# Kernel tuning notes

Hardware: AMD Instinct MI355X
Metric: run time of the kernel (lower is better)

The kernel has to match this reference:

```python
import jax, jax.numpy as jnp
import numpy as np

NUM_EXPERTS = 4096
NUM_KEYS = 64  # floor(sqrt(num_experts))
TOP_K = 16
NORM_TOPK = False
BN_EPS = 1e-5


def setup_inputs() -> dict:
    key = jax.random.key(0)
    ks = jax.random.split(key, 7)
    B, S, H, I = 2, 2048, 2048, 8192
    s = 0.02
    return {
        "hidden_states": jax.random.normal(ks[0], (B, S, H), jnp.float32),
        "router_gate_w": jax.random.normal(ks[1], (2 * NUM_KEYS, H), jnp.float32) * s,
        "down_embed": jax.random.normal(ks[2], (NUM_EXPERTS, H), jnp.float32) * s,
        "up_embed": jax.random.normal(ks[3], (NUM_EXPERTS, H), jnp.float32) * s,
        "gate_w": jax.random.normal(ks[4], (I, H), jnp.float32) * s,
        "up_w": jax.random.normal(ks[5], (I, H), jnp.float32) * s,
        "down_w": jax.random.normal(ks[6], (H, I), jnp.float32) * s,
    }


def reference(hidden_states, router_gate_w, down_embed, up_embed, gate_w, up_w, down_w):
    B, S, H = hidden_states.shape
    x = hidden_states.reshape(-1, H)  # [N, H]

    # BatchNorm1d(affine=False), training-mode batch statistics (biased var)
    mu = jnp.mean(x, axis=0, keepdims=True)
    var = jnp.mean(jnp.square(x - mu), axis=0, keepdims=True)
    xn = (x - mu) * jax.lax.rsqrt(var + BN_EPS)

    # product-key router: logits [2, N, num_keys]
    rlog = (xn @ router_gate_w.T).reshape(-1, 2, NUM_KEYS).transpose(1, 0, 2)
    logp = jax.nn.log_softmax(rlog, axis=-1)

    # full product scores [N, nk, nk]; top-k over nk*nk candidates
    full = logp[0][:, :, None] + logp[1][:, None, :]
    scores, indices = jax.lax.top_k(full.reshape(-1, NUM_KEYS * NUM_KEYS), TOP_K)
    routing_weights = jnp.exp(scores)  # [N, k]
    if NORM_TOPK:
        routing_weights = routing_weights / jnp.sum(routing_weights, axis=-1, keepdims=True)

    # PEER-style expert: scalar key match then weighted up-embedding sum
    d = down_embed[indices]  # [N, k, H]
    u = up_embed[indices]    # [N, k, H]
    h = jnp.einsum('nh,nkh->nk', x, d)
    experts_states = jnp.einsum('nk,nk,nkh->nh', routing_weights, h, u)

    # dense gated MLP (silu)
    mlp = (jax.nn.silu(x @ gate_w.T) * (x @ up_w.T)) @ down_w.T

    out = (mlp + experts_states).reshape(B, S, H)
    return out, rlog
```

## Files before the change

kernel.cpp:

```cpp
#include <hip/hip_runtime.h>
#include <stdint.h>

#define H_DIM 2048
#define N_TOK 4096
#define I_DIM 8192

typedef __attribute__((ext_vector_type(8))) short short8;
typedef __attribute__((ext_vector_type(4))) float f32x4;

typedef const __attribute__((address_space(1))) unsigned int* gp_t;
typedef __attribute__((address_space(3))) unsigned int* lp_t;

__device__ __forceinline__ void gload16(const unsigned short* g, short* l) {
    __builtin_amdgcn_global_load_lds((gp_t)g, (lp_t)l, 16, 0, 0);
}

__device__ __forceinline__ unsigned short f2bf(float f) {
    union { float f; unsigned int u; } c; c.f = f;
    unsigned int u = c.u;
    return (unsigned short)((u + 0x7FFFu + ((u >> 16) & 1u)) >> 16);
}
__device__ __forceinline__ float bf2f(unsigned short u) {
    union { unsigned int i; float f; } c; c.i = ((unsigned int)u) << 16;
    return c.f;
}

__device__ __forceinline__ float wmax64(float v) {
#pragma unroll
    for (int o = 32; o > 0; o >>= 1) v = fmaxf(v, __shfl_xor(v, o));
    return v;
}
__device__ __forceinline__ float wsum64(float v) {
#pragma unroll
    for (int o = 32; o > 0; o >>= 1) v += __shfl_xor(v, o);
    return v;
}

template<int K, int RSTEP, int LSTEP>
__device__ __forceinline__ void stage4(const unsigned short* src, short* dst) {
#pragma unroll
    for (int j = 0; j < 4; ++j)
        gload16(src + (size_t)j * RSTEP * K, dst + j * LSTEP);
}

__global__ __launch_bounds__(256) void bn_stats(const float* __restrict__ x,
                                                float* __restrict__ ps, float* __restrict__ pq) {
    int col = blockIdx.x * 256 + threadIdx.x;
    int r0  = blockIdx.y * 128;
    float s = 0.f, q = 0.f;
    for (int r = 0; r < 128; ++r) {
        float v = x[(size_t)(r0 + r) * H_DIM + col];
        s += v; q += v * v;
    }
    ps[blockIdx.y * H_DIM + col] = s;
    pq[blockIdx.y * H_DIM + col] = q;
}

__global__ __launch_bounds__(256) void bn_finalize(const float* __restrict__ ps, const float* __restrict__ pq,
                                                   float* __restrict__ mu, float* __restrict__ rsig) {
    int c = blockIdx.x * 256 + threadIdx.x;
    float s = 0.f, q = 0.f;
    for (int i = 0; i < 32; ++i) { s += ps[i * H_DIM + c]; q += pq[i * H_DIM + c]; }
    float m = s * (1.f / N_TOK);
    float v = q * (1.f / N_TOK) - m * m;
    mu[c] = m;
    rsig[c] = rsqrtf(v + 1e-5f);
}

__global__ __launch_bounds__(256) void cvt_all(const float* __restrict__ gw, const float* __restrict__ uw,
                                               const float* __restrict__ dw, const float* __restrict__ de,
                                               const float* __restrict__ ue, const float* __restrict__ x,
                                               unsigned short* __restrict__ gwb, unsigned short* __restrict__ uwb,
                                               unsigned short* __restrict__ dwb, unsigned short* __restrict__ deb,
                                               unsigned short* __restrict__ ueb, unsigned short* __restrict__ xb) {
    int b = blockIdx.x;
    const float* src; unsigned short* dst; size_t base;
    if      (b < 8192)  { src = gw; dst = gwb; base = (size_t)b; }
    else if (b < 16384) { src = uw; dst = uwb; base = (size_t)(b - 8192); }
    else if (b < 24576) { src = dw; dst = dwb; base = (size_t)(b - 16384); }
    else if (b < 28672) { src = de; dst = deb; base = (size_t)(b - 24576); }
    else if (b < 32768) { src = ue; dst = ueb; base = (size_t)(b - 28672); }
    else                { src = x;  dst = xb;  base = (size_t)(b - 32768); }
    size_t off = (base * 256 + threadIdx.x) * 8;
    float4 a = *(const float4*)(src + off);
    float4 c = *(const float4*)(src + off + 4);
    short8 s;
    s[0]=(short)f2bf(a.x); s[1]=(short)f2bf(a.y); s[2]=(short)f2bf(a.z); s[3]=(short)f2bf(a.w);
    s[4]=(short)f2bf(c.x); s[5]=(short)f2bf(c.y); s[6]=(short)f2bf(c.z); s[7]=(short)f2bf(c.w);
    *(short8*)(dst + off) = s;
}

__global__ __launch_bounds__(256) void cvt_x(const float* __restrict__ x, unsigned short* __restrict__ xb) {
    size_t i = ((size_t)blockIdx.x * 256 + threadIdx.x) * 4;
    float4 v = *(const float4*)(x + i);
    uint2 o;
    o.x = (unsigned)f2bf(v.x) | ((unsigned)f2bf(v.y) << 16);
    o.y = (unsigned)f2bf(v.z) | ((unsigned)f2bf(v.w) << 16);
    *(uint2*)(xb + i) = o;
}

__global__ __launch_bounds__(256) void cvt_w(const float* __restrict__ src, unsigned short* __restrict__ dst) {
    size_t off = ((size_t)blockIdx.x * 256 + threadIdx.x) * 8;
    float4 a = *(const float4*)(src + off);
    float4 b = *(const float4*)(src + off + 4);
    short8 s;
    s[0]=(short)f2bf(a.x); s[1]=(short)f2bf(a.y); s[2]=(short)f2bf(a.z); s[3]=(short)f2bf(a.w);
    s[4]=(short)f2bf(b.x); s[5]=(short)f2bf(b.y); s[6]=(short)f2bf(b.z); s[7]=(short)f2bf(b.w);
    *(short8*)(dst + off) = s;
}

__global__ __launch_bounds__(256) void router_kernel(const float* __restrict__ x, const float* __restrict__ rgw,
                                                     const float* __restrict__ mu, const float* __restrict__ rsig,
                                                     float* __restrict__ rlog) {
    __shared__ float xs[16][65];
    __shared__ float rs[128][65];
    const int t = threadIdx.x;
    const int n0 = blockIdx.x * 16;
    const int tk = t >> 5;
    const int jj = t & 31;
    float acc[2][4] = {{0.f,0.f,0.f,0.f},{0.f,0.f,0.f,0.f}};

    for (int kc = 0; kc < H_DIM; kc += 64) {
        {
            int row = t >> 4, c4 = (t & 15) * 4;
            float4 v = *(const float4*)(x + (size_t)(n0 + row) * H_DIM + kc + c4);
            float4 m = *(const float4*)(mu + kc + c4);
            float4 r = *(const float4*)(rsig + kc + c4);
            xs[row][c4 + 0] = (v.x - m.x) * r.x;
            xs[row][c4 + 1] = (v.y - m.y) * r.y;
            xs[row][c4 + 2] = (v.z - m.z) * r.z;
            xs[row][c4 + 3] = (v.w - m.w) * r.w;
        }
        {
            int row = t >> 1, base = (t & 1) * 32;
            const float* src = rgw + (size_t)row * H_DIM + kc + base;
#pragma unroll
            for (int i = 0; i < 8; ++i) {
                float4 v = *(const float4*)(src + i * 4);
                rs[row][base + i*4 + 0] = v.x;
                rs[row][base + i*4 + 1] = v.y;
                rs[row][base + i*4 + 2] = v.z;
                rs[row][base + i*4 + 3] = v.w;
            }
        }
        __syncthreads();
#pragma unroll 4
        for (int k = 0; k < 64; ++k) {
            float x0 = xs[tk][k], x1 = xs[tk + 8][k];
            float r0 = rs[jj][k], r1 = rs[jj + 32][k], r2 = rs[jj + 64][k], r3 = rs[jj + 96][k];
            acc[0][0] += x0 * r0; acc[0][1] += x0 * r1; acc[0][2] += x0 * r2; acc[0][3] += x0 * r3;
            acc[1][0] += x1 * r0; acc[1][1] += x1 * r1; acc[1][2] += x1 * r2; acc[1][3] += x1 * r3;
        }
        __syncthreads();
    }
#pragma unroll
    for (int a = 0; a < 2; ++a)
#pragma unroll
        for (int b = 0; b < 4; ++b) {
            int n = n0 + tk + 8 * a;
            int j = jj + 32 * b;
            rlog[(size_t)(j >> 6) * (N_TOK * 64) + (size_t)n * 64 + (j & 63)] = acc[a][b];
        }
}

__global__ __launch_bounds__(256) void topk_kernel(const float* __restrict__ rlog,
                                                   float* __restrict__ topw, int* __restrict__ topi) {
    const int lane = threadIdx.x & 63;
    const int n = blockIdx.x * 4 + (threadIdx.x >> 6);

    float a = rlog[(size_t)n * 64 + lane];
    float b = rlog[(size_t)(N_TOK * 64) + (size_t)n * 64 + lane];
    float ma = wmax64(a);
    float lpa = a - ma - logf(wsum64(expf(a - ma)));
    float mb = wmax64(b);
    float lpb = b - mb - logf(wsum64(expf(b - mb)));

    float va = lpa, vb = lpb;
    float tva = -1e30f, tvb = -1e30f; int tia = 0, tib = 0;
    for (int it = 0; it < 16; ++it) {
        float mx = wmax64(va);
        int w = __ffsll(__ballot(va == mx)) - 1;
        if (lane == it) { tva = mx; tia = w; }
        if (lane == w) va = -1e30f;
        mx = wmax64(vb);
        w = __ffsll(__ballot(vb == mx)) - 1;
        if (lane == it) { tvb = mx; tib = w; }
        if (lane == w) vb = -1e30f;
    }
    float av = __shfl(tva, lane >> 2);
    int   ai = __shfl(tia, lane >> 2);
    int   q0 = (lane & 3) * 4;
    float c0 = av + __shfl(tvb, q0 + 0); int b0 = __shfl(tib, q0 + 0);
    float c1 = av + __shfl(tvb, q0 + 1); int b1 = __shfl(tib, q0 + 1);
    float c2 = av + __shfl(tvb, q0 + 2); int b2 = __shfl(tib, q0 + 2);
    float c3 = av + __shfl(tvb, q0 + 3); int b3 = __shfl(tib, q0 + 3);

    for (int it = 0; it < 16; ++it) {
        float lv = c0; int lq = 0;
        if (c1 > lv) { lv = c1; lq = 1; }
        if (c2 > lv) { lv = c2; lq = 2; }
        if (c3 > lv) { lv = c3; lq = 3; }
        float mx = wmax64(lv);
        int w = __ffsll(__ballot(lv == mx)) - 1;
        if (lane == w) {
            int bj;
            switch (lq) {
                case 0:  bj = b0; c0 = -1e30f; break;
                case 1:  bj = b1; c1 = -1e30f; break;
                case 2:  bj = b2; c2 = -1e30f; break;
                default: bj = b3; c3 = -1e30f; break;
            }
            topw[n * 16 + it] = expf(mx);
            topi[n * 16 + it] = ai * 64 + bj;
        }
    }
}

__global__ __launch_bounds__(256) void experts_kernel_b(const float* __restrict__ x, const unsigned short* __restrict__ de,
                                                        const unsigned short* __restrict__ ue, const float* __restrict__ topw,
                                                        const int* __restrict__ topi, float* __restrict__ out) {
    __shared__ float psum[16][4];
    const int n = blockIdx.x;
    const int t = threadIdx.x, lane = t & 63, wid = t >> 6;

    float xr[8];
    {
        float4 v0 = *(const float4*)(x + (size_t)n * H_DIM + t * 8);
        float4 v1 = *(const float4*)(x + (size_t)n * H_DIM + t * 8 + 4);
        xr[0]=v0.x; xr[1]=v0.y; xr[2]=v0.z; xr[3]=v0.w;
        xr[4]=v1.x; xr[5]=v1.y; xr[6]=v1.z; xr[7]=v1.w;
    }
    int   eidx[16];
    float ew[16];
#pragma unroll
    for (int k = 0; k < 16; ++k) { eidx[k] = topi[n * 16 + k]; ew[k] = topw[n * 16 + k]; }

#pragma unroll
    for (int k = 0; k < 16; ++k) {
        short8 d = *(const short8*)(de + (size_t)eidx[k] * H_DIM + t * 8);
        float p = 0.f;
#pragma unroll
        for (int j = 0; j < 8; ++j) p += bf2f((unsigned short)d[j]) * xr[j];
        p = wsum64(p);
        if (lane == 0) psum[k][wid] = p;
    }
    __syncthreads();

    float acc[8] = {0,0,0,0,0,0,0,0};
#pragma unroll
    for (int k = 0; k < 16; ++k) {
        float h = psum[k][0] + psum[k][1] + psum[k][2] + psum[k][3];
        float coef = ew[k] * h;
        short8 u = *(const short8*)(ue + (size_t)eidx[k] * H_DIM + t * 8);
#pragma unroll
        for (int j = 0; j < 8; ++j) acc[j] += coef * bf2f((unsigned short)u[j]);
    }
    float4 o0 = {acc[0], acc[1], acc[2], acc[3]};
    float4 o1 = {acc[4], acc[5], acc[6], acc[7]};
    *(float4*)(out + (size_t)n * H_DIM + t * 8)     = o0;
    *(float4*)(out + (size_t)n * H_DIM + t * 8 + 4) = o1;
}

__global__ __launch_bounds__(256) void experts_kernel(const float* __restrict__ x, const float* __restrict__ de,
                                                      const float* __restrict__ ue, const float* __restrict__ topw,
                                                      const int* __restrict__ topi, float* __restrict__ out) {
    __shared__ float psum[16][4];
    const int n = blockIdx.x;
    const int t = threadIdx.x, lane = t & 63, wid = t >> 6;

    float xr[8];
    {
        float4 v0 = *(const float4*)(x + (size_t)n * H_DIM + t * 8);
        float4 v1 = *(const float4*)(x + (size_t)n * H_DIM + t * 8 + 4);
        xr[0]=v0.x; xr[1]=v0.y; xr[2]=v0.z; xr[3]=v0.w;
        xr[4]=v1.x; xr[5]=v1.y; xr[6]=v1.z; xr[7]=v1.w;
    }
    int   eidx[16];
    float ew[16];
#pragma unroll
    for (int k = 0; k < 16; ++k) { eidx[k] = topi[n * 16 + k]; ew[k] = topw[n * 16 + k]; }

#pragma unroll
    for (int k = 0; k < 16; ++k) {
        const float* dr = de + (size_t)eidx[k] * H_DIM + t * 8;
        float4 v0 = *(const float4*)dr;
        float4 v1 = *(const float4*)(dr + 4);
        float p = v0.x*xr[0] + v0.y*xr[1] + v0.z*xr[2] + v0.w*xr[3]
                + v1.x*xr[4] + v1.y*xr[5] + v1.z*xr[6] + v1.w*xr[7];
        p = wsum64(p);
        if (lane == 0) psum[k][wid] = p;
    }
    __syncthreads();

    float acc[8] = {0,0,0,0,0,0,0,0};
#pragma unroll
    for (int k = 0; k < 16; ++k) {
        float h = psum[k][0] + psum[k][1] + psum[k][2] + psum[k][3];
        float coef = ew[k] * h;
        const float* ur = ue + (size_t)eidx[k] * H_DIM + t * 8;
        float4 v0 = *(const float4*)ur;
        float4 v1 = *(const float4*)(ur + 4);
        acc[0] += coef * v0.x; acc[1] += coef * v0.y; acc[2] += coef * v0.z; acc[3] += coef * v0.w;
        acc[4] += coef * v1.x; acc[5] += coef * v1.y; acc[6] += coef * v1.z; acc[7] += coef * v1.w;
    }
    float4 o0 = {acc[0], acc[1], acc[2], acc[3]};
    float4 o1 = {acc[4], acc[5], acc[6], acc[7]};
    *(float4*)(out + (size_t)n * H_DIM + t * 8)     = o0;
    *(float4*)(out + (size_t)n * H_DIM + t * 8 + 4) = o1;
}

#define SWZB(row, byteoff) ((byteoff) ^ (((row) & 7) << 4))

#define NT256 (H_DIM / 64)

__global__ __launch_bounds__(512, 2) void gemm256(const unsigned short* __restrict__ Amat,
                                                  const unsigned short* __restrict__ Bmat,
                                                  unsigned short* __restrict__ act, int mode) {
    __shared__ __attribute__((aligned(16))) short sA[2][16384];
    __shared__ __attribute__((aligned(16))) short sB[2][16384];
    const int t = threadIdx.x;
    const int lane = t & 63, wid = t >> 6;
    const int wm = wid >> 2, wn = wid & 3;
    const int l15 = lane & 15, l4 = lane >> 4;
    const int bid = blockIdx.x;
    const int sw = (bid & 7) * 64 + (bid >> 3);
    const int bx = sw & 31, by = sw >> 5;
    const int row0 = by * 256, col0 = bx * 256;

    const int rseg = lane >> 3;
    const int chunk = (lane & 7) ^ rseg;
    const unsigned short* aSrc = Amat + (size_t)(row0 + wid * 8 + rseg) * H_DIM + chunk * 8;
    const unsigned short* bSrc = Bmat + (size_t)(col0 + wid * 8 + rseg) * H_DIM + chunk * 8;

    const int swzb = (l15 & 7) << 4;
    const int kx0 = (l4 * 16) ^ swzb;
    const int kx1 = (64 + l4 * 16) ^ swzb;
    const int arow = (wm * 128 + l15) * 64;
    const int brow = (wn * 64 + l15) * 64;

    f32x4 zero = {0.f, 0.f, 0.f, 0.f};
    f32x4 acc[8][4];
#pragma unroll
    for (int m = 0; m < 8; ++m)
#pragma unroll
        for (int n = 0; n < 4; ++n) acc[m][n] = zero;

    stage4<H_DIM, 64, 4096>(aSrc, &sA[0][wid * 512]);
    stage4<H_DIM, 64, 4096>(bSrc, &sB[0][wid * 512]);
    __syncthreads();

    int cur = 0;
    for (int g = 0; g < NT256; ++g) {
        if (g + 1 < NT256) {
            stage4<H_DIM, 64, 4096>(aSrc + (size_t)(g + 1) * 64, &sA[cur ^ 1][wid * 512]);
            stage4<H_DIM, 64, 4096>(bSrc + (size_t)(g + 1) * 64, &sB[cur ^ 1][wid * 512]);
        }
        const short* Ac = &sA[cur][0];
        const short* Bc = &sB[cur][0];
        {
            short8 a0[4], a0h[4], b0[4];
#pragma unroll
            for (int m = 0; m < 4; ++m) a0[m]  = *(const short8*)(Ac + arow + m * 1024 + (kx0 >> 1));
#pragma unroll
            for (int m = 0; m < 4; ++m) a0h[m] = *(const short8*)(Ac + arow + (m + 4) * 1024 + (kx0 >> 1));
#pragma unroll
            for (int n = 0; n < 4; ++n) b0[n]  = *(const short8*)(Bc + brow + n * 1024 + (kx0 >> 1));
            __builtin_amdgcn_s_setprio(1);
#pragma unroll
            for (int m = 0; m < 4; ++m)
#pragma unroll
                for (int n = 0; n < 4; ++n)
                    acc[m][n] = __builtin_amdgcn_mfma_f32_16x16x32_bf16(a0[m], b0[n], acc[m][n], 0, 0, 0);
#pragma unroll
            for (int m = 0; m < 4; ++m)
#pragma unroll
                for (int n = 0; n < 4; ++n)
                    acc[m + 4][n] = __builtin_amdgcn_mfma_f32_16x16x32_bf16(a0h[m], b0[n], acc[m + 4][n], 0, 0, 0);
            __builtin_amdgcn_s_setprio(0);
        }
        {
            short8 a1[4], a1h[4], b1[4];
#pragma unroll
            for (int m = 0; m < 4; ++m) a1[m]  = *(const short8*)(Ac + arow + m * 1024 + (kx1 >> 1));
#pragma unroll
            for (int m = 0; m < 4; ++m) a1h[m] = *(const short8*)(Ac + arow + (m + 4) * 1024 + (kx1 >> 1));
#pragma unroll
            for (int n = 0; n < 4; ++n) b1[n]  = *(const short8*)(Bc + brow + n * 1024 + (kx1 >> 1));
            __builtin_amdgcn_s_setprio(1);
#pragma unroll
            for (int m = 0; m < 4; ++m)
#pragma unroll
                for (int n = 0; n < 4; ++n)
                    acc[m][n] = __builtin_amdgcn_mfma_f32_16x16x32_bf16(a1[m], b1[n], acc[m][n], 0, 0, 0);
#pragma unroll
            for (int m = 0; m < 4; ++m)
#pragma unroll
                for (int n = 0; n < 4; ++n)
                    acc[m + 4][n] = __builtin_amdgcn_mfma_f32_16x16x32_bf16(a1h[m], b1[n], acc[m + 4][n], 0, 0, 0);
            __builtin_amdgcn_s_setprio(0);
        }
        __syncthreads();
        cur ^= 1;
    }

    const int rbase = row0 + wm * 128, cbase = col0 + wn * 64;
    if (mode == 0) {
#pragma unroll
        for (int m = 0; m < 8; ++m)
#pragma unroll
            for (int n = 0; n < 4; ++n)
#pragma unroll
                for (int j = 0; j < 4; ++j) {
                    int r = rbase + m * 16 + l4 * 4 + j;
                    int c2 = cbase + n * 16 + l15;
                    act[(size_t)r * I_DIM + c2] = f2bf(acc[m][n][j]);
                }
    } else {
#pragma unroll
        for (int m = 0; m < 8; ++m)
#pragma unroll
            for (int n = 0; n < 4; ++n)
#pragma unroll
                for (int j = 0; j < 4; ++j) {
                    int r = rbase + m * 16 + l4 * 4 + j;
                    int c2 = cbase + n * 16 + l15;
                    size_t idx = (size_t)r * I_DIM + c2;
                    float gv = bf2f(act[idx]);
                    float uv = acc[m][n][j];
                    float sv = gv / (1.f + expf(-gv));
                    act[idx] = f2bf(sv * uv);
                }
    }
}

#define NTD (I_DIM / 64)

__global__ __launch_bounds__(256, 2) void gemm_down128(const unsigned short* __restrict__ act,
                                                       const unsigned short* __restrict__ dwb,
                                                       float* __restrict__ out) {
    __shared__ __attribute__((aligned(16))) short sA[2][8192];
    __shared__ __attribute__((aligned(16))) short sB[2][8192];
    const int t = threadIdx.x;
    const int lane = t & 63, wid = t >> 6;
    const int wm = wid >> 1, wn = wid & 1;
    const int l15 = lane & 15, l4 = lane >> 4;
    const int bid = blockIdx.x;
    const int sw = (bid & 7) * 64 + (bid >> 3);
    const int bx = sw & 15, by = sw >> 4;
    const int row0 = by * 128, col0 = bx * 128;

    const int rseg = lane >> 3;
    const int chunk = (lane & 7) ^ rseg;
    const unsigned short* aSrc = act + (size_t)(row0 + wid * 8 + rseg) * I_DIM + chunk * 8;
    const unsigned short* bSrc = dwb + (size_t)(col0 + wid * 8 + rseg) * I_DIM + chunk * 8;

    const int swzb = (l15 & 7) << 4;
    const int kx0 = (l4 * 16) ^ swzb;
    const int kx1 = (64 + l4 * 16) ^ swzb;
    const int arow = (wm * 64 + l15) * 64;
    const int brow = (wn * 64 + l15) * 64;

    f32x4 zero = {0.f, 0.f, 0.f, 0.f};
    f32x4 acc[4][4];
#pragma unroll
    for (int m = 0; m < 4; ++m)
#pragma unroll
        for (int n = 0; n < 4; ++n) acc[m][n] = zero;

    stage4<I_DIM, 32, 2048>(aSrc, &sA[0][wid * 512]);
    stage4<I_DIM, 32, 2048>(bSrc, &sB[0][wid * 512]);
    __syncthreads();

    int cur = 0;
    for (int g = 0; g < NTD; ++g) {
        if (g + 1 < NTD) {
            stage4<I_DIM, 32, 2048>(aSrc + (size_t)(g + 1) * 64, &sA[cur ^ 1][wid * 512]);
            stage4<I_DIM, 32, 2048>(bSrc + (size_t)(g + 1) * 64, &sB[cur ^ 1][wid * 512]);
        }
        const short* Ac = &sA[cur][0];
        const short* Bc = &sB[cur][0];
        {
            short8 a0[4], b0[4];
#pragma unroll
            for (int m = 0; m < 4; ++m) a0[m] = *(const short8*)(Ac + arow + m * 1024 + (kx0 >> 1));
#pragma unroll
            for (int n = 0; n < 4; ++n) b0[n] = *(const short8*)(Bc + brow + n * 1024 + (kx0 >> 1));
            __builtin_amdgcn_s_setprio(1);
#pragma unroll
            for (int m = 0; m < 4; ++m)
#pragma unroll
                for (int n = 0; n < 4; ++n)
                    acc[m][n] = __builtin_amdgcn_mfma_f32_16x16x32_bf16(a0[m], b0[n], acc[m][n], 0, 0, 0);
            __builtin_amdgcn_s_setprio(0);
        }
        {
            short8 a1[4], b1[4];
#pragma unroll
            for (int m = 0; m < 4; ++m) a1[m] = *(const short8*)(Ac + arow + m * 1024 + (kx1 >> 1));
#pragma unroll
            for (int n = 0; n < 4; ++n) b1[n] = *(const short8*)(Bc + brow + n * 1024 + (kx1 >> 1));
            __builtin_amdgcn_s_setprio(1);
#pragma unroll
            for (int m = 0; m < 4; ++m)
#pragma unroll
                for (int n = 0; n < 4; ++n)
                    acc[m][n] = __builtin_amdgcn_mfma_f32_16x16x32_bf16(a1[m], b1[n], acc[m][n], 0, 0, 0);
            __builtin_amdgcn_s_setprio(0);
        }
        __syncthreads();
        cur ^= 1;
    }

    const int rbase = row0 + wm * 64, cbase = col0 + wn * 64;
#pragma unroll
    for (int m = 0; m < 4; ++m)
#pragma unroll
        for (int n = 0; n < 4; ++n)
#pragma unroll
            for (int j = 0; j < 4; ++j) {
                int r = rbase + m * 16 + l4 * 4 + j;
                int c2 = cbase + n * 16 + l15;
                out[(size_t)r * H_DIM + c2] += acc[m][n][j];
            }
}

__global__ __launch_bounds__(256) void gemm_gu(const unsigned short* __restrict__ xb,
                                               const float* __restrict__ gw, const float* __restrict__ uw,
                                               unsigned short* __restrict__ act) {
    __shared__ __attribute__((aligned(16))) short As[128 * 64];
    __shared__ __attribute__((aligned(16))) short Bg[128 * 64];
    __shared__ __attribute__((aligned(16))) short Bu[128 * 64];
    const int t = threadIdx.x;
    const int lane = t & 63, wid = t >> 6;
    const int wr = wid >> 1, wc = wid & 1;
    const int l15 = lane & 15, l4 = lane >> 4;
    const int row0 = blockIdx.y * 128;
    const int col0 = blockIdx.x * 128;
    const int srow = t >> 1, shalf = (t & 1) * 32;

    f32x4 zero = {0.f, 0.f, 0.f, 0.f};
    f32x4 accg[4][4], accu[4][4];
#pragma unroll
    for (int m = 0; m < 4; ++m)
#pragma unroll
        for (int n = 0; n < 4; ++n) { accg[m][n] = zero; accu[m][n] = zero; }

    for (int kt = 0; kt < H_DIM; kt += 64) {
        {
            const unsigned short* src = xb + (size_t)(row0 + srow) * H_DIM + kt + shalf;
#pragma unroll
            for (int i = 0; i < 4; ++i) {
                int boff = SWZB(srow, (shalf + i * 8) * 2);
                *(short8*)(As + srow * 64 + (boff >> 1)) = *(const short8*)(src + i * 8);
            }
        }
        {
            const float* g = gw + (size_t)(col0 + srow) * H_DIM + kt + shalf;
            const float* u = uw + (size_t)(col0 + srow) * H_DIM + kt + shalf;
#pragma unroll
            for (int i = 0; i < 4; ++i) {
                int boff = SWZB(srow, (shalf + i * 8) * 2);
                float4 a0 = *(const float4*)(g + i * 8);
                float4 a1 = *(const float4*)(g + i * 8 + 4);
                short8 s;
                s[0]=(short)f2bf(a0.x); s[1]=(short)f2bf(a0.y); s[2]=(short)f2bf(a0.z); s[3]=(short)f2bf(a0.w);
                s[4]=(short)f2bf(a1.x); s[5]=(short)f2bf(a1.y); s[6]=(short)f2bf(a1.z); s[7]=(short)f2bf(a1.w);
                *(short8*)(Bg + srow * 64 + (boff >> 1)) = s;
                float4 b0 = *(const float4*)(u + i * 8);
                float4 b1 = *(const float4*)(u + i * 8 + 4);
                short8 r;
                r[0]=(short)f2bf(b0.x); r[1]=(short)f2bf(b0.y); r[2]=(short)f2bf(b0.z); r[3]=(short)f2bf(b0.w);
                r[4]=(short)f2bf(b1.x); r[5]=(short)f2bf(b1.y); r[6]=(short)f2bf(b1.z); r[7]=(short)f2bf(b1.w);
                *(short8*)(Bu + srow * 64 + (boff >> 1)) = r;
            }
        }
        __syncthreads();
#pragma unroll
        for (int kk = 0; kk < 64; kk += 32) {
            short8 af[4], bgf[4], buf_[4];
#pragma unroll
            for (int m = 0; m < 4; ++m) {
                int row = wr * 64 + m * 16 + l15;
                af[m] = *(const short8*)(As + row * 64 + (SWZB(row, (kk + l4 * 8) * 2) >> 1));
            }
#pragma unroll
            for (int n = 0; n < 4; ++n) {
                int row = wc * 64 + n * 16 + l15;
                int off = row * 64 + (SWZB(row, (kk + l4 * 8) * 2) >> 1);
                bgf[n]  = *(const short8*)(Bg + off);
                buf_[n] = *(const short8*)(Bu + off);
            }
#pragma unroll
            for (int m = 0; m < 4; ++m)
#pragma unroll
                for (int n = 0; n < 4; ++n) {
                    accg[m][n] = __builtin_amdgcn_mfma_f32_16x16x32_bf16(af[m], bgf[n],  accg[m][n], 0, 0, 0);
                    accu[m][n] = __builtin_amdgcn_mfma_f32_16x16x32_bf16(af[m], buf_[n], accu[m][n], 0, 0, 0);
                }
        }
        __syncthreads();
    }
    const int rbase = row0 + wr * 64, cbase = col0 + wc * 64;
#pragma unroll
    for (int m = 0; m < 4; ++m)
#pragma unroll
        for (int n = 0; n < 4; ++n)
#pragma unroll
            for (int j = 0; j < 4; ++j) {
                int r = rbase + m * 16 + l4 * 4 + j;
                int c = cbase + n * 16 + l15;
                float gv = accg[m][n][j];
                float uv = accu[m][n][j];
                float sv = gv / (1.f + expf(-gv));
                act[(size_t)r * I_DIM + c] = f2bf(sv * uv);
            }
}

__global__ __launch_bounds__(256) void gemm_down(const unsigned short* __restrict__ act,
                                                 const float* __restrict__ dw, float* __restrict__ out) {
    __shared__ __attribute__((aligned(16))) short As[128 * 64];
    __shared__ __attribute__((aligned(16))) short Bs[128 * 64];
    const int t = threadIdx.x;
    const int lane = t & 63, wid = t >> 6;
    const int wr = wid >> 1, wc = wid & 1;
    const int l15 = lane & 15, l4 = lane >> 4;
    const int row0 = blockIdx.y * 128;
    const int col0 = blockIdx.x * 128;
    const int srow = t >> 1, shalf = (t & 1) * 32;

    f32x4 zero = {0.f, 0.f, 0.f, 0.f};
    f32x4 acc[4][4];
#pragma unroll
    for (int m = 0; m < 4; ++m)
#pragma unroll
        for (int n = 0; n < 4; ++n) acc[m][n] = zero;

    for (int kt = 0; kt < I_DIM; kt += 64) {
        {
            const unsigned short* src = act + (size_t)(row0 + srow) * I_DIM + kt + shalf;
#pragma unroll
            for (int i = 0; i < 4; ++i) {
                int boff = SWZB(srow, (shalf + i * 8) * 2);
                *(short8*)(As + srow * 64 + (boff >> 1)) = *(const short8*)(src + i * 8);
            }
        }
        {
            const float* g = dw + (size_t)(col0 + srow) * I_DIM + kt + shalf;
#pragma unroll
            for (int i = 0; i < 4; ++i) {
                int boff = SWZB(srow, (shalf + i * 8) * 2);
                float4 a0 = *(const float4*)(g + i * 8);
                float4 a1 = *(const float4*)(g + i * 8 + 4);
                short8 s;
                s[0]=(short)f2bf(a0.x); s[1]=(short)f2bf(a0.y); s[2]=(short)f2bf(a0.z); s[3]=(short)f2bf(a0.w);
                s[4]=(short)f2bf(a1.x); s[5]=(short)f2bf(a1.y); s[6]=(short)f2bf(a1.z); s[7]=(short)f2bf(a1.w);
                *(short8*)(Bs + srow * 64 + (boff >> 1)) = s;
            }
        }
        __syncthreads();
#pragma unroll
        for (int kk = 0; kk < 64; kk += 32) {
            short8 af[4], bf[4];
#pragma unroll
            for (int m = 0; m < 4; ++m) {
                int row = wr * 64 + m * 16 + l15;
                af[m] = *(const short8*)(As + row * 64 + (SWZB(row, (kk + l4 * 8) * 2) >> 1));
            }
#pragma unroll
            for (int n = 0; n < 4; ++n) {
                int row = wc * 64 + n * 16 + l15;
                bf[n] = *(const short8*)(Bs + row * 64 + (SWZB(row, (kk + l4 * 8) * 2) >> 1));
            }
#pragma unroll
            for (int m = 0; m < 4; ++m)
#pragma unroll
                for (int n = 0; n < 4; ++n)
                    acc[m][n] = __builtin_amdgcn_mfma_f32_16x16x32_bf16(af[m], bf[n], acc[m][n], 0, 0, 0);
        }
        __syncthreads();
    }
    const int rbase = row0 + wr * 64, cbase = col0 + wc * 64;
#pragma unroll
    for (int m = 0; m < 4; ++m)
#pragma unroll
        for (int n = 0; n < 4; ++n)
#pragma unroll
            for (int j = 0; j < 4; ++j) {
                int r = rbase + m * 16 + l4 * 4 + j;
                int c = cbase + n * 16 + l15;
                out[(size_t)r * H_DIM + c] += acc[m][n][j];
            }
}

extern "C" void kernel_launch(void* const* d_in, const int* in_sizes, int n_in,
                              void* d_out, int out_size, void* d_ws, size_t ws_size,
                              hipStream_t stream) {
    const float* x   = (const float*)d_in[0];
    const float* rgw = (const float*)d_in[1];
    const float* de  = (const float*)d_in[2];
    const float* ue  = (const float*)d_in[3];
    const float* gw  = (const float*)d_in[4];
    const float* uw  = (const float*)d_in[5];
    const float* dw  = (const float*)d_in[6];
    float* out = (float*)d_out;
    char* ws = (char*)d_ws;

    float* ps   = (float*)(ws + 0);
    float* pq   = (float*)(ws + 262144);
    float* mu   = (float*)(ws + 524288);
    float* rsig = (float*)(ws + 532480);
    float* topw = (float*)(ws + 540672);
    int*   topi = (int*)  (ws + 802816);
    unsigned short* xb  = (unsigned short*)(ws + 1179648);
    unsigned short* act = (unsigned short*)(ws + 17956864);
    unsigned short* gwb = (unsigned short*)(ws + 85065728);
    unsigned short* uwb = (unsigned short*)(ws + 118620160);
    unsigned short* dwb = (unsigned short*)(ws + 152174592);
    unsigned short* deb = (unsigned short*)(ws + 185729024);
    unsigned short* ueb = (unsigned short*)(ws + 202506240);
    float* rlog = out + 8388608;
    const bool fast  = ws_size >= 185729024ULL;
    const bool fast2 = ws_size >= 219283456ULL;

    bn_stats   <<<dim3(8, 32), 256, 0, stream>>>(x, ps, pq);
    bn_finalize<<<8, 256, 0, stream>>>(ps, pq, mu, rsig);
    router_kernel<<<256, 256, 0, stream>>>(x, rgw, mu, rsig, rlog);
    topk_kernel<<<1024, 256, 0, stream>>>(rlog, topw, topi);

    if (fast2) {
        cvt_all<<<36864, 256, 0, stream>>>(gw, uw, dw, de, ue, x, gwb, uwb, dwb, deb, ueb, xb);
        experts_kernel_b<<<4096, 256, 0, stream>>>(x, deb, ueb, topw, topi, out);
        gemm256<<<512, 512, 0, stream>>>(xb, gwb, act, 0);
        gemm256<<<512, 512, 0, stream>>>(xb, uwb, act, 1);
        gemm_down128<<<512, 256, 0, stream>>>(act, dwb, out);
    } else if (fast) {
        cvt_x<<<8192, 256, 0, stream>>>(x, xb);
        cvt_w<<<8192, 256, 0, stream>>>(gw, gwb);
        cvt_w<<<8192, 256, 0, stream>>>(uw, uwb);
        cvt_w<<<8192, 256, 0, stream>>>(dw, dwb);
        experts_kernel<<<4096, 256, 0, stream>>>(x, de, ue, topw, topi, out);
        gemm256<<<512, 512, 0, stream>>>(xb, gwb, act, 0);
        gemm256<<<512, 512, 0, stream>>>(xb, uwb, act, 1);
        gemm_down128<<<512, 256, 0, stream>>>(act, dwb, out);
    } else {
        cvt_x<<<8192, 256, 0, stream>>>(x, xb);
        experts_kernel<<<4096, 256, 0, stream>>>(x, de, ue, topw, topi, out);
        gemm_gu  <<<dim3(64, 32), 256, 0, stream>>>(xb, gw, uw, act);
        gemm_down<<<dim3(16, 32), 256, 0, stream>>>(act, dw, out);
    }
}
```

Measured before the change: 768.9 us.

## Fuse gate and up GEMMs into one kernel with SiLU epilogue

```diff
diff --git a/kernel.cpp b/kernel.cpp
--- a/kernel.cpp
+++ b/kernel.cpp
@@ -40,6 +40,12 @@
 __device__ __forceinline__ void stage4(const unsigned short* src, short* dst) {
 #pragma unroll
     for (int j = 0; j < 4; ++j)
+        gload16(src + (size_t)j * RSTEP * K, dst + j * LSTEP);
+}
+template<int K, int RSTEP, int LSTEP>
+__device__ __forceinline__ void stage2(const unsigned short* src, short* dst) {
+#pragma unroll
+    for (int j = 0; j < 2; ++j)
         gload16(src + (size_t)j * RSTEP * K, dst + j * LSTEP);
 }
 
@@ -311,126 +317,112 @@
 
 #define SWZB(row, byteoff) ((byteoff) ^ (((row) & 7) << 4))
 
-#define NT256 (H_DIM / 64)
-
-__global__ __launch_bounds__(512, 2) void gemm256(const unsigned short* __restrict__ Amat,
-                                                  const unsigned short* __restrict__ Bmat,
-                                                  unsigned short* __restrict__ act, int mode) {
+#define NTGU (H_DIM / 64)
+
+__global__ __launch_bounds__(512, 2) void gemm_gu256(const unsigned short* __restrict__ xb,
+                                                     const unsigned short* __restrict__ gwb,
+                                                     const unsigned short* __restrict__ uwb,
+                                                     unsigned short* __restrict__ act) {
     __shared__ __attribute__((aligned(16))) short sA[2][16384];
-    __shared__ __attribute__((aligned(16))) short sB[2][16384];
+    __shared__ __attribute__((aligned(16))) short sBg[2][8192];
+    __shared__ __attribute__((aligned(16))) short sBu[2][8192];
     const int t = threadIdx.x;
     const int lane = t & 63, wid = t >> 6;
-    const int wm = wid >> 2, wn = wid & 3;
+    const int wm = wid >> 1, wn = wid & 1;
     const int l15 = lane & 15, l4 = lane >> 4;
     const int bid = blockIdx.x;
-    const int sw = (bid & 7) * 64 + (bid >> 3);
-    const int bx = sw & 31, by = sw >> 5;
-    const int row0 = by * 256, col0 = bx * 256;
+    const int sw = (bid & 7) * 128 + (bid >> 3);
+    const int bx = sw & 63, by = sw >> 6;
+    const int row0 = by * 256, col0 = bx * 128;
 
     const int rseg = lane >> 3;
     const int chunk = (lane & 7) ^ rseg;
-    const unsigned short* aSrc = Amat + (size_t)(row0 + wid * 8 + rseg) * H_DIM + chunk * 8;
-    const unsigned short* bSrc = Bmat + (size_t)(col0 + wid * 8 + rseg) * H_DIM + chunk * 8;
+    const unsigned short* aSrc = xb  + (size_t)(row0 + wid * 8 + rseg) * H_DIM + chunk * 8;
+    const unsigned short* gSrc = gwb + (size_t)(col0 + wid * 8 + rseg) * H_DIM + chunk * 8;
+    const unsigned short* uSrc = uwb + (size_t)(col0 + wid * 8 + rseg) * H_DIM + chunk * 8;
 
     const int swzb = (l15 & 7) << 4;
     const int kx0 = (l4 * 16) ^ swzb;
     const int kx1 = (64 + l4 * 16) ^ swzb;
-    const int arow = (wm * 128 + l15) * 64;
+    const int arow = (wm * 64 + l15) * 64;
     const int brow = (wn * 64 + l15) * 64;
 
     f32x4 zero = {0.f, 0.f, 0.f, 0.f};
-    f32x4 acc[8][4];
-#pragma unroll
-    for (int m = 0; m < 8; ++m)
-#pragma unroll
-        for (int n = 0; n < 4; ++n) acc[m][n] = zero;
+    f32x4 accg[4][4], accu[4][4];
+#pragma unroll
+    for (int m = 0; m < 4; ++m)
+#pragma unroll
+        for (int n = 0; n < 4; ++n) { accg[m][n] = zero; accu[m][n] = zero; }
 
     stage4<H_DIM, 64, 4096>(aSrc, &sA[0][wid * 512]);
-    stage4<H_DIM, 64, 4096>(bSrc, &sB[0][wid * 512]);
+    stage2<H_DIM, 64, 4096>(gSrc, &sBg[0][wid * 512]);
+    stage2<H_DIM, 64, 4096>(uSrc, &sBu[0][wid * 512]);
     __syncthreads();
 
     int cur = 0;
-    for (int g = 0; g < NT256; ++g) {
-        if (g + 1 < NT256) {
+    for (int g = 0; g < NTGU; ++g) {
+        if (g + 1 < NTGU) {
             stage4<H_DIM, 64, 4096>(aSrc + (size_t)(g + 1) * 64, &sA[cur ^ 1][wid * 512]);
-            stage4<H_DIM, 64, 4096>(bSrc + (size_t)(g + 1) * 64, &sB[cur ^ 1][wid * 512]);
+            stage2<H_DIM, 64, 4096>(gSrc + (size_t)(g + 1) * 64, &sBg[cur ^ 1][wid * 512]);
+            stage2<H_DIM, 64, 4096>(uSrc + (size_t)(g + 1) * 64, &sBu[cur ^ 1][wid * 512]);
         }
         const short* Ac = &sA[cur][0];
-        const short* Bc = &sB[cur][0];
-        {
-            short8 a0[4], a0h[4], b0[4];
+        const short* Gc = &sBg[cur][0];
+        const short* Uc = &sBu[cur][0];
+        {
+            short8 a0[4], bg0[4], bu0[4];
 #pragma unroll
             for (int m = 0; m < 4; ++m) a0[m]  = *(const short8*)(Ac + arow + m * 1024 + (kx0 >> 1));
 #pragma unroll
-            for (int m = 0; m < 4; ++m) a0h[m] = *(const short8*)(Ac + arow + (m + 4) * 1024 + (kx0 >> 1));
-#pragma unroll
-            for (int n = 0; n < 4; ++n) b0[n]  = *(const short8*)(Bc + brow + n * 1024 + (kx0 >> 1));
+            for (int n = 0; n < 4; ++n) bg0[n] = *(const short8*)(Gc + brow + n * 1024 + (kx0 >> 1));
+#pragma unroll
+            for (int n = 0; n < 4; ++n) bu0[n] = *(const short8*)(Uc + brow + n * 1024 + (kx0 >> 1));
             __builtin_amdgcn_s_setprio(1);
 #pragma unroll
             for (int m = 0; m < 4; ++m)
 #pragma unroll
-                for (int n = 0; n < 4; ++n)
-                    acc[m][n] = __builtin_amdgcn_mfma_f32_16x16x32_bf16(a0[m], b0[n], acc[m][n], 0, 0, 0);
+                for (int n = 0; n < 4; ++n) {
+                    accg[m][n] = __builtin_amdgcn_mfma_f32_16x16x32_bf16(a0[m], bg0[n], accg[m][n], 0, 0, 0);
+                    accu[m][n] = __builtin_amdgcn_mfma_f32_16x16x32_bf16(a0[m], bu0[n], accu[m][n], 0, 0, 0);
+                }
+            __builtin_amdgcn_s_setprio(0);
+        }
+        {
+            short8 a1[4], bg1[4], bu1[4];
+#pragma unroll
+            for (int m = 0; m < 4; ++m) a1[m]  = *(const short8*)(Ac + arow + m * 1024 + (kx1 >> 1));
+#pragma unroll
+            for (int n = 0; n < 4; ++n) bg1[n] = *(const short8*)(Gc + brow + n * 1024 + (kx1 >> 1));
+#pragma unroll
+            for (int n = 0; n < 4; ++n) bu1[n] = *(const short8*)(Uc + brow + n * 1024 + (kx1 >> 1));
+            __builtin_amdgcn_s_setprio(1);
 #pragma unroll
             for (int m = 0; m < 4; ++m)
 #pragma unroll
-                for (int n = 0; n < 4; ++n)
-                    acc[m + 4][n] = __builtin_amdgcn_mfma_f32_16x16x32_bf16(a0h[m], b0[n], acc[m + 4][n], 0, 0, 0);
-            __builtin_amdgcn_s_setprio(0);
-        }
-        {
-            short8 a1[4], a1h[4], b1[4];
-#pragma unroll
-            for (int m = 0; m < 4; ++m) a1[m]  = *(const short8*)(Ac + arow + m * 1024 + (kx1 >> 1));
-#pragma unroll
-            for (int m = 0; m < 4; ++m) a1h[m] = *(const short8*)(Ac + arow + (m + 4) * 1024 + (kx1 >> 1));
-#pragma unroll
-            for (int n = 0; n < 4; ++n) b1[n]  = *(const short8*)(Bc + brow + n * 1024 + (kx1 >> 1));
-            __builtin_amdgcn_s_setprio(1);
-#pragma unroll
-            for (int m = 0; m < 4; ++m)
-#pragma unroll
-                for (int n = 0; n < 4; ++n)
-                    acc[m][n] = __builtin_amdgcn_mfma_f32_16x16x32_bf16(a1[m], b1[n], acc[m][n], 0, 0, 0);
-#pragma unroll
-            for (int m = 0; m < 4; ++m)
-#pragma unroll
-                for (int n = 0; n < 4; ++n)
-                    acc[m + 4][n] = __builtin_amdgcn_mfma_f32_16x16x32_bf16(a1h[m], b1[n], acc[m + 4][n], 0, 0, 0);
+                for (int n = 0; n < 4; ++n) {
+                    accg[m][n] = __builtin_amdgcn_mfma_f32_16x16x32_bf16(a1[m], bg1[n], accg[m][n], 0, 0, 0);
+                    accu[m][n] = __builtin_amdgcn_mfma_f32_16x16x32_bf16(a1[m], bu1[n], accu[m][n], 0, 0, 0);
+                }
             __builtin_amdgcn_s_setprio(0);
         }
         __syncthreads();
         cur ^= 1;
     }
 
-    const int rbase = row0 + wm * 128, cbase = col0 + wn * 64;
-    if (mode == 0) {
-#pragma unroll
-        for (int m = 0; m < 8; ++m)
-#pragma unroll
-            for (int n = 0; n < 4; ++n)
-#pragma unroll
-                for (int j = 0; j < 4; ++j) {
-                    int r = rbase + m * 16 + l4 * 4 + j;
-                    int c2 = cbase + n * 16 + l15;
-                    act[(size_t)r * I_DIM + c2] = f2bf(acc[m][n][j]);
-                }
-    } else {
-#pragma unroll
-        for (int m = 0; m < 8; ++m)
-#pragma unroll
-            for (int n = 0; n < 4; ++n)
-#pragma unroll
-                for (int j = 0; j < 4; ++j) {
-                    int r = rbase + m * 16 + l4 * 4 + j;
-                    int c2 = cbase + n * 16 + l15;
-                    size_t idx = (size_t)r * I_DIM + c2;
-                    float gv = bf2f(act[idx]);
-                    float uv = acc[m][n][j];
-                    float sv = gv / (1.f + expf(-gv));
-                    act[idx] = f2bf(sv * uv);
-                }
-    }
+    const int rbase = row0 + wm * 64, cbase = col0 + wn * 64;
+#pragma unroll
+    for (int m = 0; m < 4; ++m)
+#pragma unroll
+        for (int n = 0; n < 4; ++n)
+#pragma unroll
+            for (int j = 0; j < 4; ++j) {
+                int r = rbase + m * 16 + l4 * 4 + j;
+                int c2 = cbase + n * 16 + l15;
+                float gv = accg[m][n][j];
+                float uv = accu[m][n][j];
+                float sv = gv / (1.f + expf(-gv));
+                act[(size_t)r * I_DIM + c2] = f2bf(sv * uv);
+            }
 }
 
 #define NTD (I_DIM / 64)
@@ -730,8 +722,7 @@
     if (fast2) {
         cvt_all<<<36864, 256, 0, stream>>>(gw, uw, dw, de, ue, x, gwb, uwb, dwb, deb, ueb, xb);
         experts_kernel_b<<<4096, 256, 0, stream>>>(x, deb, ueb, topw, topi, out);
-        gemm256<<<512, 512, 0, stream>>>(xb, gwb, act, 0);
-        gemm256<<<512, 512, 0, stream>>>(xb, uwb, act, 1);
+        gemm_gu256<<<1024, 512, 0, stream>>>(xb, gwb, uwb, act);
         gemm_down128<<<512, 256, 0, stream>>>(act, dwb, out);
     } else if (fast) {
         cvt_x<<<8192, 256, 0, stream>>>(x, xb);
@@ -739,8 +730,7 @@
         cvt_w<<<8192, 256, 0, stream>>>(uw, uwb);
         cvt_w<<<8192, 256, 0, stream>>>(dw, dwb);
         experts_kernel<<<4096, 256, 0, stream>>>(x, de, ue, topw, topi, out);
-        gemm256<<<512, 512, 0, stream>>>(xb, gwb, act, 0);
-        gemm256<<<512, 512, 0, stream>>>(xb, uwb, act, 1);
+        gemm_gu256<<<1024, 512, 0, stream>>>(xb, gwb, uwb, act);
         gemm_down128<<<512, 256, 0, stream>>>(act, dwb, out);
     } else {
         cvt_x<<<8192, 256, 0, stream>>>(x, xb);
```

After: 756.1 us. Within noise of the previous version (-1.7%).
